# Optimization experiments

Hardware: AMD Instinct MI355X
Metric: run time of the kernel (lower is better)

The kernel has to match this reference:

```python
import jax, jax.numpy as jnp
import numpy as np

N_HEAD = 16
LORA_SCALE = 1.0 / 4.0  # alpha=1, r=4
LN_EPS = 1e-5


def _ln(x, g, b):
    # LayerNorm subclass casts to float32 then back to input dtype
    xf = x.astype(jnp.float32)
    m = xf.mean(-1, keepdims=True)
    v = xf.var(-1, keepdims=True)
    y = (xf - m) / jnp.sqrt(v + LN_EPS) * g + b
    return y.astype(x.dtype)


def _lora(h, a, b):
    # x @ a.T @ b.T * scaling ; a:[r,d], b:[d,r]
    return (h @ a.T) @ b.T * LORA_SCALE


def _attn(h, Wq, bq, Wk, Wv, bv, Wo, bo, la_k, lb_k, la_v, lb_v, la_o, lb_o):
    B, S, D = h.shape
    hd = D // N_HEAD
    scale = hd ** (-0.25)
    q = h @ Wq.T + bq
    k = h @ Wk.T + _lora(h, la_k, lb_k)          # key Linear has no bias
    v = h @ Wv.T + bv + _lora(h, la_v, lb_v)
    qh = q.reshape(B, S, N_HEAD, hd).transpose(0, 2, 1, 3) * scale  # [B,H,S,hd]
    kh = k.reshape(B, S, N_HEAD, hd).transpose(0, 2, 1, 3) * scale
    vh = v.reshape(B, S, N_HEAD, hd).transpose(0, 2, 1, 3)
    qk = jnp.einsum('bhqd,bhkd->bhqk', qh, kh).astype(jnp.float32)
    w = jax.nn.softmax(qk, axis=-1).astype(q.dtype)
    wv = jnp.einsum('bhqk,bhkd->bhqd', w, vh)
    wv = wv.transpose(0, 2, 1, 3).reshape(B, S, D)
    return wv @ Wo.T + bo + _lora(wv, la_o, lb_o)


def setup_inputs() -> dict:
    key = jax.random.key(0)
    D, R = 1024, 4
    B, S = 8, 1024
    ks = jax.random.split(key, 20)
    sd = 0.02
    inp = {
        'x': jax.random.normal(ks[0], (B, S, D), jnp.float32),
        'Wq': jax.random.normal(ks[1], (D, D), jnp.float32) * sd,
        'bq': jnp.zeros((D,), jnp.float32),
        'Wk': jax.random.normal(ks[2], (D, D), jnp.float32) * sd,
        'Wv': jax.random.normal(ks[3], (D, D), jnp.float32) * sd,
        'bv': jnp.zeros((D,), jnp.float32),
        'Wo': jax.random.normal(ks[4], (D, D), jnp.float32) * sd,
        'bo': jnp.zeros((D,), jnp.float32),
        'la_k': jax.random.normal(ks[5], (R, D), jnp.float32) * sd,
        'lb_k': jax.random.normal(ks[6], (D, R), jnp.float32) * sd,
        'la_v': jax.random.normal(ks[7], (R, D), jnp.float32) * sd,
        'lb_v': jax.random.normal(ks[8], (D, R), jnp.float32) * sd,
        'la_o': jax.random.normal(ks[9], (R, D), jnp.float32) * sd,
        'lb_o': jax.random.normal(ks[10], (D, R), jnp.float32) * sd,
        'g_attn': jnp.ones((D,), jnp.float32),
        'b_attn': jnp.zeros((D,), jnp.float32),
        'W1': jax.random.normal(ks[11], (4 * D, D), jnp.float32) * sd,
        'b1': jnp.zeros((4 * D,), jnp.float32),
        'W2': jax.random.normal(ks[12], (D, 4 * D), jnp.float32) * sd,
        'b2': jnp.zeros((D,), jnp.float32),
        'g_mlp': jnp.ones((D,), jnp.float32),
        'b_mlp': jnp.zeros((D,), jnp.float32),
    }
    return inp


def reference(x, Wq, bq, Wk, Wv, bv, Wo, bo, la_k, lb_k, la_v, lb_v, la_o, lb_o,
              g_attn, b_attn, W1, b1, W2, b2, g_mlp, b_mlp):
    # self-attention + residual (LoRA on key/value/out)
    x = x + _attn(_ln(x, g_attn, b_attn), Wq, bq, Wk, Wv, bv, Wo, bo,
                  la_k, lb_k, la_v, lb_v, la_o, lb_o)
    # MLP + residual (exact GELU, matching nn.GELU default)
    h = _ln(x, g_mlp, b_mlp)
    h = jax.nn.gelu(h @ W1.T + b1, approximate=False)
    x = x + h @ W2.T + b2
    return x
```

## Files before the change

### kernel.cpp

```cpp
#include <hip/hip_runtime.h>
#include <math.h>

typedef _Float16 f16_t;
typedef f16_t f16x8 __attribute__((ext_vector_type(8)));
typedef f16_t f16x4 __attribute__((ext_vector_type(4)));
typedef float f32x4 __attribute__((ext_vector_type(4)));
typedef float fv4 __attribute__((ext_vector_type(4)));

#define MFMA16(a, b, c) __builtin_amdgcn_mfma_f32_16x16x32_f16(a, b, c, 0, 0, 0)

__device__ __forceinline__ void gload16(const void* g, void* l) {
  __builtin_amdgcn_global_load_lds((const __attribute__((address_space(1))) void*)g,
                                   (__attribute__((address_space(3))) void*)l, 16, 0, 0);
}

__global__ __launch_bounds__(256) void ln_f32(const float* __restrict__ x,
                                              const float* __restrict__ g,
                                              const float* __restrict__ b,
                                              f16_t* __restrict__ y) {
  const int D = 1024;
  int row = blockIdx.x;
  int t = threadIdx.x;
  const float* xr = x + (size_t)row * D + t * 4;
  float x0 = xr[0], x1 = xr[1], x2 = xr[2], x3 = xr[3];
  float sum = x0 + x1 + x2 + x3;
  float sq = x0 * x0 + x1 * x1 + x2 * x2 + x3 * x3;
  for (int d = 32; d; d >>= 1) {
    sum += __shfl_down(sum, d);
    sq += __shfl_down(sq, d);
  }
  __shared__ float ssum[4], ssq[4];
  int w = t >> 6, lane = t & 63;
  if (lane == 0) { ssum[w] = sum; ssq[w] = sq; }
  __syncthreads();
  float ts = ssum[0] + ssum[1] + ssum[2] + ssum[3];
  float tq = ssq[0] + ssq[1] + ssq[2] + ssq[3];
  float mean = ts * (1.0f / 1024.0f);
  float var = tq * (1.0f / 1024.0f) - mean * mean;
  float rstd = rsqrtf(var + 1e-5f);
  f16_t* yr = y + (size_t)row * D + t * 4;
  const float* gr = g + t * 4;
  const float* br = b + t * 4;
  yr[0] = (f16_t)((x0 - mean) * rstd * gr[0] + br[0]);
  yr[1] = (f16_t)((x1 - mean) * rstd * gr[1] + br[1]);
  yr[2] = (f16_t)((x2 - mean) * rstd * gr[2] + br[2]);
  yr[3] = (f16_t)((x3 - mean) * rstd * gr[3] + br[3]);
}

__global__ __launch_bounds__(256) void ln_f16(const f16_t* __restrict__ x,
                                              const float* __restrict__ g,
                                              const float* __restrict__ b,
                                              f16_t* __restrict__ y) {
  const int D = 1024;
  int row = blockIdx.x;
  int t = threadIdx.x;
  const f16_t* xr = x + (size_t)row * D + t * 4;
  float x0 = (float)xr[0], x1 = (float)xr[1], x2 = (float)xr[2], x3 = (float)xr[3];
  float sum = x0 + x1 + x2 + x3;
  float sq = x0 * x0 + x1 * x1 + x2 * x2 + x3 * x3;
  for (int d = 32; d; d >>= 1) {
    sum += __shfl_down(sum, d);
    sq += __shfl_down(sq, d);
  }
  __shared__ float ssum[4], ssq[4];
  int w = t >> 6, lane = t & 63;
  if (lane == 0) { ssum[w] = sum; ssq[w] = sq; }
  __syncthreads();
  float ts = ssum[0] + ssum[1] + ssum[2] + ssum[3];
  float tq = ssq[0] + ssq[1] + ssq[2] + ssq[3];
  float mean = ts * (1.0f / 1024.0f);
  float var = tq * (1.0f / 1024.0f) - mean * mean;
  float rstd = rsqrtf(var + 1e-5f);
  f16_t* yr = y + (size_t)row * D + t * 4;
  const float* gr = g + t * 4;
  const float* br = b + t * 4;
  yr[0] = (f16_t)((x0 - mean) * rstd * gr[0] + br[0]);
  yr[1] = (f16_t)((x1 - mean) * rstd * gr[1] + br[1]);
  yr[2] = (f16_t)((x2 - mean) * rstd * gr[2] + br[2]);
  yr[3] = (f16_t)((x3 - mean) * rstd * gr[3] + br[3]);
}

__global__ __launch_bounds__(256) void convert_w(
    const float* __restrict__ wq, const float* __restrict__ wk,
    const float* __restrict__ wv, const float* __restrict__ wo,
    const float* __restrict__ w1, const float* __restrict__ w2,
    f16_t* __restrict__ oq, f16_t* __restrict__ ok, f16_t* __restrict__ ov,
    f16_t* __restrict__ oo, f16_t* __restrict__ o1, f16_t* __restrict__ o2) {
  int bid = blockIdx.x;
  const float* src;
  f16_t* dst;
  int bi;
  if (bid < 2048) {
    int seg = bid >> 9;
    bi = bid & 511;
    src = seg == 0 ? wq : seg == 1 ? wk : seg == 2 ? wv : wo;
    dst = seg == 0 ? oq : seg == 1 ? ok : seg == 2 ? ov : oo;
  } else if (bid < 4096) {
    bi = bid - 2048; src = w1; dst = o1;
  } else {
    bi = bid - 4096; src = w2; dst = o2;
  }
  size_t idx = (size_t)bi * 2048 + (size_t)threadIdx.x * 8;
  fv4 a = *(const fv4*)(src + idx);
  fv4 b = *(const fv4*)(src + idx + 4);
  f16x8 h;
#pragma unroll
  for (int j = 0; j < 4; ++j) { h[j] = (f16_t)a[j]; h[4 + j] = (f16_t)b[j]; }
  *(f16x8*)(dst + idx) = h;
}

__global__ __launch_bounds__(256) void lora_t_kernel(const f16_t* __restrict__ h,
                                                     const float* __restrict__ la,
                                                     float* __restrict__ t, int K) {
  int lane = threadIdx.x & 63;
  int w = threadIdx.x >> 6;
  int row = blockIdx.x * 4 + w;
  const f16_t* hrow = h + (size_t)row * K;
  float acc[4] = {0.f, 0.f, 0.f, 0.f};
  for (int it = 0; it < K / 512; ++it) {
    int base = it * 512 + lane * 8;
    f16x8 hx = *(const f16x8*)(hrow + base);
#pragma unroll
    for (int r = 0; r < 4; ++r) {
      const float* ar = la + (size_t)r * K + base;
#pragma unroll
      for (int j = 0; j < 8; ++j) acc[r] += (float)hx[j] * ar[j];
    }
  }
#pragma unroll
  for (int r = 0; r < 4; ++r) {
    for (int d = 32; d; d >>= 1) acc[r] += __shfl_down(acc[r], d);
  }
  if (lane == 0) {
#pragma unroll
    for (int r = 0; r < 4; ++r) t[(size_t)row * 4 + r] = acc[r];
  }
}

__global__ __launch_bounds__(256, 2) void gemm_f16(
    const f16_t* __restrict__ A, const f16_t* __restrict__ B,
    const float* __restrict__ bias, const float* __restrict__ loraT,
    const float* __restrict__ loraB, const float* residf,
    const f16_t* __restrict__ residb, f16_t* Cb, float* Cf, f16_t* Cvt,
    int M, int N, int K, int ldb, int dogelu) {
  __shared__ __align__(16) f16_t smem[2][16384];
  const int tid = threadIdx.x;
  const int lane = tid & 63, wid = tid >> 6;
  const int wm = wid >> 1, wn = wid & 1;
  const int l15 = lane & 15, lhi = lane >> 4;
  int nwg = gridDim.x * gridDim.y;
  int bid = blockIdx.y * gridDim.x + blockIdx.x;
  int swz = (bid & 7) * (nwg >> 3) + (bid >> 3);
  const int m0 = (swz / gridDim.x) * 128, n0 = (swz % gridDim.x) * 128;
  const int arow = tid >> 3;
  const int aslot = tid & 7;

  f32x4 acc[4][4];
#pragma unroll
  for (int i = 0; i < 4; ++i)
#pragma unroll
    for (int j = 0; j < 4; ++j) acc[i][j] = (f32x4){0.f, 0.f, 0.f, 0.f};

  auto stage = [&](const f16_t* G, int r0, int ldg, int step, char* lds) {
#pragma unroll
    for (int c = 0; c < 4; ++c) {
      int r = c * 32 + arow;
      int cm = aslot ^ (r & 7);
      gload16(G + (size_t)(r0 + r) * ldg + (size_t)step * 64 + cm * 8,
              lds + c * 4096 + wid * 1024);
    }
  };

  const int nsteps = K >> 6;
  stage(A, m0, K, 0, (char*)&smem[0][0]);
  stage(B, n0, ldb, 0, (char*)&smem[0][8192]);
  __syncthreads();
  for (int t = 0; t < nsteps; ++t) {
    int cur = t & 1, nxt = cur ^ 1;
    if (t + 1 < nsteps) {
      stage(A, m0, K, t + 1, (char*)&smem[nxt][0]);
      stage(B, n0, ldb, t + 1, (char*)&smem[nxt][8192]);
    }
    const char* As = (const char*)&smem[cur][0];
    const char* Bs = (const char*)&smem[cur][8192];
#pragma unroll
    for (int kk = 0; kk < 2; ++kk) {
      f16x8 af[4], bf[4];
#pragma unroll
      for (int i = 0; i < 4; ++i) {
        int row = wm * 64 + i * 16 + l15;
        af[i] = *(const f16x8*)(As + row * 128 + ((kk * 64 + lhi * 16) ^ ((row & 7) << 4)));
      }
#pragma unroll
      for (int j = 0; j < 4; ++j) {
        int row = wn * 64 + j * 16 + l15;
        bf[j] = *(const f16x8*)(Bs + row * 128 + ((kk * 64 + lhi * 16) ^ ((row & 7) << 4)));
      }
#pragma unroll
      for (int i = 0; i < 4; ++i)
#pragma unroll
        for (int j = 0; j < 4; ++j) acc[i][j] = MFMA16(af[i], bf[j], acc[i][j]);
    }
    __syncthreads();
  }

  const int gm = m0 + wm * 64, gn = n0 + wn * 64;
#pragma unroll
  for (int j = 0; j < 4; ++j) {
    int gcol = gn + j * 16 + l15;
    float bj = bias ? bias[gcol] : 0.f;
    float lb0 = 0.f, lb1 = 0.f, lb2 = 0.f, lb3 = 0.f;
    if (loraB) {
      const float* p = loraB + (size_t)gcol * 4;
      lb0 = p[0]; lb1 = p[1]; lb2 = p[2]; lb3 = p[3];
    }
#pragma unroll
    for (int i = 0; i < 4; ++i) {
      float v4[4];
#pragma unroll
      for (int r = 0; r < 4; ++r) {
        int grow = gm + i * 16 + lhi * 4 + r;
        float val = acc[i][j][r] + bj;
        if (loraT) {
          const float* tp = loraT + (size_t)grow * 4;
          val += 0.25f * (tp[0] * lb0 + tp[1] * lb1 + tp[2] * lb2 + tp[3] * lb3);
        }
        if (dogelu) val = 0.5f * val * (1.0f + erff(val * 0.70710678118654752f));
        if (residf) val += residf[(size_t)grow * N + gcol];
        if (residb) val += (float)residb[(size_t)grow * N + gcol];
        v4[r] = val;
      }
      if (Cf) {
#pragma unroll
        for (int r = 0; r < 4; ++r)
          Cf[(size_t)(gm + i * 16 + lhi * 4 + r) * N + gcol] = v4[r];
      } else if (Cvt) {
        int grow0 = gm + i * 16 + lhi * 4;
        int bb = grow0 >> 10, ss = grow0 & 1023;
        int hh = gcol >> 6, dd = gcol & 63;
        f16x4 pk;
#pragma unroll
        for (int r = 0; r < 4; ++r) pk[r] = (f16_t)v4[r];
        *(f16x4*)(Cvt + (((size_t)bb * 16 + hh) * 64 + dd) * 1024 + ss) = pk;
      } else {
#pragma unroll
        for (int r = 0; r < 4; ++r)
          Cb[(size_t)(gm + i * 16 + lhi * 4 + r) * N + gcol] = (f16_t)v4[r];
      }
    }
  }
}

__global__ __launch_bounds__(256, 2) void gemm_mfma(
    const f16_t* __restrict__ A, const float* __restrict__ B,
    const float* __restrict__ bias, const float* __restrict__ loraT,
    const float* __restrict__ loraB, const float* residf,
    const f16_t* __restrict__ residb, f16_t* Cb, float* Cf, f16_t* Cvt,
    int M, int N, int K, int ldb, int dogelu) {
  __shared__ __align__(16) f16_t smem[2][16384];
  const int tid = threadIdx.x;
  const int lane = tid & 63, wid = tid >> 6;
  const int wm = wid >> 1, wn = wid & 1;
  const int l15 = lane & 15, lhi = lane >> 4;
  const int m0 = blockIdx.y * 128, n0 = blockIdx.x * 128;
  const int arow = tid >> 3;
  const int aslot = tid & 7;

  f32x4 acc[4][4];
#pragma unroll
  for (int i = 0; i < 4; ++i)
#pragma unroll
    for (int j = 0; j < 4; ++j) acc[i][j] = (f32x4){0.f, 0.f, 0.f, 0.f};

  fv4 breg[4][2];

  auto stageA = [&](int step, int buf) {
#pragma unroll
    for (int c = 0; c < 4; ++c) {
      int r = c * 32 + arow;
      int cm = aslot ^ (r & 7);
      gload16(A + (size_t)(m0 + r) * K + (size_t)step * 64 + cm * 8,
              (char*)&smem[buf][0] + c * 4096 + wid * 1024);
    }
  };
  auto loadB = [&](int step) {
#pragma unroll
    for (int c = 0; c < 4; ++c) {
      int r = c * 32 + arow;
      const float* gp = B + (size_t)(n0 + r) * ldb + (size_t)step * 64 + aslot * 8;
      breg[c][0] = *(const fv4*)gp;
      breg[c][1] = *(const fv4*)(gp + 4);
    }
  };
  auto writeB = [&](int buf) {
#pragma unroll
    for (int c = 0; c < 4; ++c) {
      int r = c * 32 + arow;
      f16x8 hh;
#pragma unroll
      for (int j = 0; j < 4; ++j) hh[j] = (f16_t)breg[c][0][j];
#pragma unroll
      for (int j = 0; j < 4; ++j) hh[4 + j] = (f16_t)breg[c][1][j];
      int boff = r * 128 + ((aslot * 16) ^ ((r & 7) << 4));
      *(f16x8*)((char*)&smem[buf][8192] + boff) = hh;
    }
  };

  const int nsteps = K >> 6;
  stageA(0, 0);
  loadB(0);
  writeB(0);
  __syncthreads();
  for (int t = 0; t < nsteps; ++t) {
    int cur = t & 1, nxt = cur ^ 1;
    if (t + 1 < nsteps) { stageA(t + 1, nxt); loadB(t + 1); }
    const char* As = (const char*)&smem[cur][0];
    const char* Bs = (const char*)&smem[cur][8192];
#pragma unroll
    for (int kk = 0; kk < 2; ++kk) {
      f16x8 af[4], bf[4];
#pragma unroll
      for (int i = 0; i < 4; ++i) {
        int row = wm * 64 + i * 16 + l15;
        af[i] = *(const f16x8*)(As + row * 128 + ((kk * 64 + lhi * 16) ^ ((row & 7) << 4)));
      }
#pragma unroll
      for (int j = 0; j < 4; ++j) {
        int row = wn * 64 + j * 16 + l15;
        bf[j] = *(const f16x8*)(Bs + row * 128 + ((kk * 64 + lhi * 16) ^ ((row & 7) << 4)));
      }
#pragma unroll
      for (int i = 0; i < 4; ++i)
#pragma unroll
        for (int j = 0; j < 4; ++j) acc[i][j] = MFMA16(af[i], bf[j], acc[i][j]);
    }
    if (t + 1 < nsteps) writeB(nxt);
    __syncthreads();
  }

  const int gm = m0 + wm * 64, gn = n0 + wn * 64;
#pragma unroll
  for (int j = 0; j < 4; ++j) {
    int gcol = gn + j * 16 + l15;
    float bj = bias ? bias[gcol] : 0.f;
    float lb0 = 0.f, lb1 = 0.f, lb2 = 0.f, lb3 = 0.f;
    if (loraB) {
      const float* p = loraB + (size_t)gcol * 4;
      lb0 = p[0]; lb1 = p[1]; lb2 = p[2]; lb3 = p[3];
    }
#pragma unroll
    for (int i = 0; i < 4; ++i) {
      float v4[4];
#pragma unroll
      for (int r = 0; r < 4; ++r) {
        int grow = gm + i * 16 + lhi * 4 + r;
        float val = acc[i][j][r] + bj;
        if (loraT) {
          const float* tp = loraT + (size_t)grow * 4;
          val += 0.25f * (tp[0] * lb0 + tp[1] * lb1 + tp[2] * lb2 + tp[3] * lb3);
        }
        if (dogelu) val = 0.5f * val * (1.0f + erff(val * 0.70710678118654752f));
        if (residf) val += residf[(size_t)grow * N + gcol];
        if (residb) val += (float)residb[(size_t)grow * N + gcol];
        v4[r] = val;
      }
      if (Cf) {
#pragma unroll
        for (int r = 0; r < 4; ++r)
          Cf[(size_t)(gm + i * 16 + lhi * 4 + r) * N + gcol] = v4[r];
      } else if (Cvt) {
        int grow0 = gm + i * 16 + lhi * 4;
        int bb = grow0 >> 10, ss = grow0 & 1023;
        int hh = gcol >> 6, dd = gcol & 63;
        f16x4 pk;
#pragma unroll
        for (int r = 0; r < 4; ++r) pk[r] = (f16_t)v4[r];
        *(f16x4*)(Cvt + (((size_t)bb * 16 + hh) * 64 + dd) * 1024 + ss) = pk;
      } else {
#pragma unroll
        for (int r = 0; r < 4; ++r)
          Cb[(size_t)(gm + i * 16 + lhi * 4 + r) * N + gcol] = (f16_t)v4[r];
      }
    }
  }
}

__global__ __launch_bounds__(256, 3) void attn_mfma(const f16_t* __restrict__ q,
                                                    const f16_t* __restrict__ k,
                                                    const f16_t* __restrict__ vt,
                                                    f16_t* __restrict__ wv) {
  const int S = 1024, D = 1024;
  __shared__ __align__(16) f16_t Qs[128 * 64];
  __shared__ __align__(16) f16_t SP[128 * 64];
  __shared__ __align__(16) f16_t Ks[64 * 64];
  __shared__ __align__(16) f16_t Vts[64 * 64];
  __shared__ float rsb[128];
  __shared__ float lib[128];
  const int tid = threadIdx.x, lane = tid & 63, w = tid >> 6;
  const int l15 = lane & 15, lhi = lane >> 4;
  const int q0 = blockIdx.x * 128;
  const int h = blockIdx.y, b = blockIdx.z;
  const f16_t* qg = q + ((size_t)b * S + q0) * D + h * 64;
  const f16_t* kg = k + (size_t)b * S * D + h * 64;
  const f16_t* vg = vt + ((size_t)b * 16 + h) * 64 * (size_t)S;

#pragma unroll
  for (int c = 0; c < 4; ++c) {
    int r = c * 32 + (tid >> 3), kc = tid & 7;
    f16x8 xx = *(const f16x8*)(qg + (size_t)r * D + kc * 8);
    *(f16x8*)((char*)Qs + r * 128 + ((kc * 16) ^ ((r & 7) << 4))) = xx;
  }
  __syncthreads();
  f16x8 qf[2][2];
#pragma unroll
  for (int i = 0; i < 2; ++i) {
    int row = w * 32 + i * 16 + l15;
#pragma unroll
    for (int kk = 0; kk < 2; ++kk)
      qf[i][kk] = *(const f16x8*)((char*)Qs + row * 128 +
                                  ((kk * 64 + lhi * 16) ^ ((row & 7) << 4)));
  }

  f32x4 oacc[2][4];
#pragma unroll
  for (int i = 0; i < 2; ++i)
#pragma unroll
    for (int j = 0; j < 4; ++j) oacc[i][j] = (f32x4){0.f, 0.f, 0.f, 0.f};
  float m_run = -1e30f, l_run = 0.f;
  const int myrow = w * 32 + (lane >> 1);
  const int half = lane & 1;

  for (int kv = 0; kv < 16; ++kv) {
    __syncthreads();
#pragma unroll
    for (int c = 0; c < 2; ++c) {
      int r = c * 32 + (tid >> 3), kc = tid & 7;
      f16x8 xk = *(const f16x8*)(kg + (size_t)(kv * 64 + r) * D + kc * 8);
      *(f16x8*)((char*)Ks + r * 128 + ((kc * 16) ^ ((r & 7) << 4))) = xk;
      f16x8 xv = *(const f16x8*)(vg + (size_t)r * S + kv * 64 + kc * 8);
      *(f16x8*)((char*)Vts + r * 128 + ((kc * 16) ^ ((r & 7) << 4))) = xv;
    }
    __syncthreads();
    f32x4 sacc[2][4];
#pragma unroll
    for (int i = 0; i < 2; ++i)
#pragma unroll
      for (int j = 0; j < 4; ++j) sacc[i][j] = (f32x4){0.f, 0.f, 0.f, 0.f};
#pragma unroll
    for (int kk = 0; kk < 2; ++kk) {
      f16x8 kf[4];
#pragma unroll
      for (int j = 0; j < 4; ++j) {
        int row = j * 16 + l15;
        kf[j] = *(const f16x8*)((char*)Ks + row * 128 +
                                ((kk * 64 + lhi * 16) ^ ((row & 7) << 4)));
      }
#pragma unroll
      for (int i = 0; i < 2; ++i)
#pragma unroll
        for (int j = 0; j < 4; ++j) sacc[i][j] = MFMA16(qf[i][kk], kf[j], sacc[i][j]);
    }
#pragma unroll
    for (int i = 0; i < 2; ++i)
#pragma unroll
      for (int j = 0; j < 4; ++j)
#pragma unroll
        for (int r = 0; r < 4; ++r) {
          int srow = w * 32 + i * 16 + lhi * 4 + r;
          int scol = j * 16 + l15;
          *(f16_t*)((char*)SP + srow * 128 + ((scol * 2) ^ ((srow & 7) << 4))) =
              (f16_t)(sacc[i][j][r] * 0.125f);
        }
    __syncthreads();
    f16x8 ch[4];
#pragma unroll
    for (int c = 0; c < 4; ++c)
      ch[c] = *(const f16x8*)((char*)SP + myrow * 128 +
                              ((half * 64 + c * 16) ^ ((myrow & 7) << 4)));
    float mt = -1e30f;
#pragma unroll
    for (int c = 0; c < 4; ++c)
#pragma unroll
      for (int e = 0; e < 8; ++e) mt = fmaxf(mt, (float)ch[c][e]);
    mt = fmaxf(mt, __shfl_xor(mt, 1));
    float mnew = fmaxf(m_run, mt);
    float resc = __expf(m_run - mnew);
    float lsum = 0.f;
#pragma unroll
    for (int c = 0; c < 4; ++c) {
      f16x8 p8;
#pragma unroll
      for (int e = 0; e < 8; ++e) {
        float p = __expf((float)ch[c][e] - mnew);
        lsum += p;
        p8[e] = (f16_t)p;
      }
      *(f16x8*)((char*)SP + myrow * 128 + ((half * 64 + c * 16) ^ ((myrow & 7) << 4))) = p8;
    }
    lsum += __shfl_xor(lsum, 1);
    l_run = l_run * resc + lsum;
    m_run = mnew;
    if (half == 0) rsb[myrow] = resc;
    __syncthreads();
#pragma unroll
    for (int i = 0; i < 2; ++i) {
      float f0 = rsb[w * 32 + i * 16 + lhi * 4 + 0];
      float f1 = rsb[w * 32 + i * 16 + lhi * 4 + 1];
      float f2 = rsb[w * 32 + i * 16 + lhi * 4 + 2];
      float f3 = rsb[w * 32 + i * 16 + lhi * 4 + 3];
#pragma unroll
      for (int j = 0; j < 4; ++j) {
        oacc[i][j][0] *= f0;
        oacc[i][j][1] *= f1;
        oacc[i][j][2] *= f2;
        oacc[i][j][3] *= f3;
      }
    }
#pragma unroll
    for (int kk = 0; kk < 2; ++kk) {
      f16x8 pa[2], vb[4];
#pragma unroll
      for (int i = 0; i < 2; ++i) {
        int row = w * 32 + i * 16 + l15;
        pa[i] = *(const f16x8*)((char*)SP + row * 128 +
                                ((kk * 64 + lhi * 16) ^ ((row & 7) << 4)));
      }
#pragma unroll
      for (int j = 0; j < 4; ++j) {
        int row = j * 16 + l15;
        vb[j] = *(const f16x8*)((char*)Vts + row * 128 +
                                ((kk * 64 + lhi * 16) ^ ((row & 7) << 4)));
      }
#pragma unroll
      for (int i = 0; i < 2; ++i)
#pragma unroll
        for (int j = 0; j < 4; ++j) oacc[i][j] = MFMA16(pa[i], vb[j], oacc[i][j]);
    }
  }
  if (half == 0) lib[myrow] = 1.f / l_run;
  __syncthreads();
#pragma unroll
  for (int i = 0; i < 2; ++i)
#pragma unroll
    for (int r = 0; r < 4; ++r) {
      int row = w * 32 + i * 16 + lhi * 4 + r;
      float li = lib[row];
      size_t base = ((size_t)b * S + q0 + row) * D + h * 64;
#pragma unroll
      for (int j = 0; j < 4; ++j)
        wv[base + j * 16 + l15] = (f16_t)(oacc[i][j][r] * li);
    }
}

extern "C" void kernel_launch(void* const* d_in, const int* in_sizes, int n_in,
                              void* d_out, int out_size, void* d_ws, size_t ws_size,
                              hipStream_t stream) {
  const int B = 8, S = 1024, D = 1024, F = 4096;
  const int M = B * S;

  const float* x = (const float*)d_in[0];
  const float* Wq = (const float*)d_in[1];
  const float* bq = (const float*)d_in[2];
  const float* Wk = (const float*)d_in[3];
  const float* Wv = (const float*)d_in[4];
  const float* bv = (const float*)d_in[5];
  const float* Wo = (const float*)d_in[6];
  const float* bo = (const float*)d_in[7];
  const float* la_k = (const float*)d_in[8];
  const float* lb_k = (const float*)d_in[9];
  const float* la_v = (const float*)d_in[10];
  const float* lb_v = (const float*)d_in[11];
  const float* la_o = (const float*)d_in[12];
  const float* lb_o = (const float*)d_in[13];
  const float* g_attn = (const float*)d_in[14];
  const float* b_attn = (const float*)d_in[15];
  const float* W1 = (const float*)d_in[16];
  const float* b1 = (const float*)d_in[17];
  const float* W2 = (const float*)d_in[18];
  const float* b2 = (const float*)d_in[19];
  const float* g_mlp = (const float*)d_in[20];
  const float* b_mlp = (const float*)d_in[21];

  float* t_k = (float*)((char*)d_ws + 16);
  float* t_v = t_k + (size_t)M * 4;
  float* t_o = t_v + (size_t)M * 4;
  const size_t MD = (size_t)M * D;
  f16_t* P0 = (f16_t*)((char*)d_ws + 409600);
  f16_t* P1 = P0 + MD;
  f16_t* P2 = P0 + 2 * MD;
  f16_t* P3 = P0 + 3 * MD;
  f16_t* Wqf = P0 + 4 * MD;
  f16_t* Wkf = Wqf + (size_t)D * D;
  f16_t* Wvf = Wkf + (size_t)D * D;
  f16_t* Wof = Wvf + (size_t)D * D;
  f16_t* W1f = Wof + (size_t)D * D;
  f16_t* W2f = W1f + (size_t)F * D;
  float* outf = (float*)d_out;
  const size_t need = 409600 + 4 * MD * sizeof(f16_t) +
                      (4 * (size_t)D * D + 2 * (size_t)F * D) * sizeof(f16_t);
  const bool f16w = ws_size >= need;

  if (f16w)
    convert_w<<<6144, 256, 0, stream>>>(Wq, Wk, Wv, Wo, W1, W2,
                                        Wqf, Wkf, Wvf, Wof, W1f, W2f);

  ln_f32<<<M, 256, 0, stream>>>(x, g_attn, b_attn, P0);
  lora_t_kernel<<<M / 4, 256, 0, stream>>>(P0, la_k, t_k, D);
  lora_t_kernel<<<M / 4, 256, 0, stream>>>(P0, la_v, t_v, D);
  if (f16w) {
    gemm_f16<<<dim3(8, 64), 256, 0, stream>>>(
        P0, Wqf, bq, nullptr, nullptr, nullptr, nullptr, P1, nullptr, nullptr,
        M, D, D, D, 0);
    gemm_f16<<<dim3(8, 64), 256, 0, stream>>>(
        P0, Wkf, nullptr, t_k, lb_k, nullptr, nullptr, P2, nullptr, nullptr,
        M, D, D, D, 0);
    gemm_f16<<<dim3(8, 64), 256, 0, stream>>>(
        P0, Wvf, bv, t_v, lb_v, nullptr, nullptr, nullptr, nullptr, P3,
        M, D, D, D, 0);
  } else {
    gemm_mfma<<<dim3(8, 64), 256, 0, stream>>>(
        P0, Wq, bq, nullptr, nullptr, nullptr, nullptr, P1, nullptr, nullptr,
        M, D, D, D, 0);
    gemm_mfma<<<dim3(8, 64), 256, 0, stream>>>(
        P0, Wk, nullptr, t_k, lb_k, nullptr, nullptr, P2, nullptr, nullptr,
        M, D, D, D, 0);
    gemm_mfma<<<dim3(8, 64), 256, 0, stream>>>(
        P0, Wv, bv, t_v, lb_v, nullptr, nullptr, nullptr, nullptr, P3,
        M, D, D, D, 0);
  }
  attn_mfma<<<dim3(8, 16, 8), 256, 0, stream>>>(P1, P2, P3, P0);
  lora_t_kernel<<<M / 4, 256, 0, stream>>>(P0, la_o, t_o, D);
  if (f16w)
    gemm_f16<<<dim3(8, 64), 256, 0, stream>>>(
        P0, Wof, bo, t_o, lb_o, x, nullptr, P3, nullptr, nullptr, M, D, D, D, 0);
  else
    gemm_mfma<<<dim3(8, 64), 256, 0, stream>>>(
        P0, Wo, bo, t_o, lb_o, x, nullptr, P3, nullptr, nullptr, M, D, D, D, 0);
  ln_f16<<<M, 256, 0, stream>>>(P3, g_mlp, b_mlp, P0);
  if (f16w) {
    gemm_f16<<<dim3(16, 64), 256, 0, stream>>>(
        P0, W1f, b1, nullptr, nullptr, nullptr, nullptr, P1, nullptr, nullptr,
        M, 2048, D, D, 1);
    gemm_f16<<<dim3(8, 64), 256, 0, stream>>>(
        P1, W2f, b2, nullptr, nullptr, nullptr, P3, nullptr, outf, nullptr,
        M, D, 2048, F, 0);
    gemm_f16<<<dim3(16, 64), 256, 0, stream>>>(
        P0, W1f + (size_t)2048 * D, b1 + 2048, nullptr, nullptr, nullptr, nullptr,
        P1, nullptr, nullptr, M, 2048, D, D, 1);
    gemm_f16<<<dim3(8, 64), 256, 0, stream>>>(
        P1, W2f + 2048, nullptr, nullptr, nullptr, outf, nullptr, nullptr, outf,
        nullptr, M, D, 2048, F, 0);
  } else {
    gemm_mfma<<<dim3(16, 64), 256, 0, stream>>>(
        P0, W1, b1, nullptr, nullptr, nullptr, nullptr, P1, nullptr, nullptr,
        M, 2048, D, D, 1);
    gemm_mfma<<<dim3(8, 64), 256, 0, stream>>>(
        P1, W2, b2, nullptr, nullptr, nullptr, P3, nullptr, outf, nullptr,
        M, D, 2048, F, 0);
    gemm_mfma<<<dim3(16, 64), 256, 0, stream>>>(
        P0, W1 + (size_t)2048 * D, b1 + 2048, nullptr, nullptr, nullptr, nullptr,
        P1, nullptr, nullptr, M, 2048, D, D, 1);
    gemm_mfma<<<dim3(8, 64), 256, 0, stream>>>(
        P1, W2 + 2048, nullptr, nullptr, nullptr, outf, nullptr, nullptr, outf,
        nullptr, M, D, 2048, F, 0);
  }
}
```

Before: 662.5 us.

## Register-resident softmax in attention, single-buffer GEMM for occupancy, fuse LoRA K/V

The attention kernel now computes the online softmax directly on the MFMA accumulator registers, using lane shuffles for the row max and row sum. This removes the LDS round trip of scores, the extra barrier and the rescale broadcast buffers, and Q staging now reuses the P buffer to cut LDS use. setprio hints are added around the MFMA phases. The f16 GEMM drops double buffering to halve LDS and raises the launch bound to 3 blocks per SM, giving up overlap of loads and compute in exchange for occupancy. The two LoRA down-projection kernels are fused into one that reads the activations once.

```diff
diff --git a/kernel.cpp b/kernel.cpp
--- a/kernel.cpp
+++ b/kernel.cpp
@@ -109,6 +109,47 @@
   *(f16x8*)(dst + idx) = h;
 }
 
+__global__ __launch_bounds__(256) void lora_kv_kernel(
+    const f16_t* __restrict__ h, const float* __restrict__ la_k,
+    const float* __restrict__ la_v, float* __restrict__ t_k,
+    float* __restrict__ t_v, int K) {
+  int lane = threadIdx.x & 63;
+  int w = threadIdx.x >> 6;
+  int row = blockIdx.x * 4 + w;
+  const f16_t* hrow = h + (size_t)row * K;
+  float ak[4] = {0.f, 0.f, 0.f, 0.f};
+  float av[4] = {0.f, 0.f, 0.f, 0.f};
+  for (int it = 0; it < K / 512; ++it) {
+    int base = it * 512 + lane * 8;
+    f16x8 hx = *(const f16x8*)(hrow + base);
+#pragma unroll
+    for (int r = 0; r < 4; ++r) {
+      const float* kr = la_k + (size_t)r * K + base;
+      const float* vr = la_v + (size_t)r * K + base;
+#pragma unroll
+      for (int j = 0; j < 8; ++j) {
+        float hv = (float)hx[j];
+        ak[r] += hv * kr[j];
+        av[r] += hv * vr[j];
+      }
+    }
+  }
+#pragma unroll
+  for (int r = 0; r < 4; ++r) {
+    for (int d = 32; d; d >>= 1) {
+      ak[r] += __shfl_down(ak[r], d);
+      av[r] += __shfl_down(av[r], d);
+    }
+  }
+  if (lane == 0) {
+#pragma unroll
+    for (int r = 0; r < 4; ++r) {
+      t_k[(size_t)row * 4 + r] = ak[r];
+      t_v[(size_t)row * 4 + r] = av[r];
+    }
+  }
+}
+
 __global__ __launch_bounds__(256) void lora_t_kernel(const f16_t* __restrict__ h,
                                                      const float* __restrict__ la,
                                                      float* __restrict__ t, int K) {
@@ -137,13 +178,14 @@
   }
 }
 
-__global__ __launch_bounds__(256, 2) void gemm_f16(
+__global__ __launch_bounds__(256, 3) void gemm_f16(
     const f16_t* __restrict__ A, const f16_t* __restrict__ B,
     const float* __restrict__ bias, const float* __restrict__ loraT,
     const float* __restrict__ loraB, const float* residf,
     const f16_t* __restrict__ residb, f16_t* Cb, float* Cf, f16_t* Cvt,
     int M, int N, int K, int ldb, int dogelu) {
-  __shared__ __align__(16) f16_t smem[2][16384];
+  __shared__ __align__(16) f16_t Asm[8192];
+  __shared__ __align__(16) f16_t Bsm[8192];
   const int tid = threadIdx.x;
   const int lane = tid & 63, wid = tid >> 6;
   const int wm = wid >> 1, wn = wid & 1;
@@ -172,36 +214,31 @@
   };
 
   const int nsteps = K >> 6;
-  stage(A, m0, K, 0, (char*)&smem[0][0]);
-  stage(B, n0, ldb, 0, (char*)&smem[0][8192]);
-  __syncthreads();
   for (int t = 0; t < nsteps; ++t) {
-    int cur = t & 1, nxt = cur ^ 1;
-    if (t + 1 < nsteps) {
-      stage(A, m0, K, t + 1, (char*)&smem[nxt][0]);
-      stage(B, n0, ldb, t + 1, (char*)&smem[nxt][8192]);
-    }
-    const char* As = (const char*)&smem[cur][0];
-    const char* Bs = (const char*)&smem[cur][8192];
+    if (t) __syncthreads();
+    stage(A, m0, K, t, (char*)Asm);
+    stage(B, n0, ldb, t, (char*)Bsm);
+    __syncthreads();
 #pragma unroll
     for (int kk = 0; kk < 2; ++kk) {
       f16x8 af[4], bf[4];
 #pragma unroll
       for (int i = 0; i < 4; ++i) {
         int row = wm * 64 + i * 16 + l15;
-        af[i] = *(const f16x8*)(As + row * 128 + ((kk * 64 + lhi * 16) ^ ((row & 7) << 4)));
+        af[i] = *(const f16x8*)((char*)Asm + row * 128 +
+                                ((kk * 64 + lhi * 16) ^ ((row & 7) << 4)));
       }
 #pragma unroll
       for (int j = 0; j < 4; ++j) {
         int row = wn * 64 + j * 16 + l15;
-        bf[j] = *(const f16x8*)(Bs + row * 128 + ((kk * 64 + lhi * 16) ^ ((row & 7) << 4)));
+        bf[j] = *(const f16x8*)((char*)Bsm + row * 128 +
+                                ((kk * 64 + lhi * 16) ^ ((row & 7) << 4)));
       }
 #pragma unroll
       for (int i = 0; i < 4; ++i)
 #pragma unroll
         for (int j = 0; j < 4; ++j) acc[i][j] = MFMA16(af[i], bf[j], acc[i][j]);
     }
-    __syncthreads();
   }
 
   const int gm = m0 + wm * 64, gn = n0 + wn * 64;
@@ -390,12 +427,9 @@
                                                     const f16_t* __restrict__ vt,
                                                     f16_t* __restrict__ wv) {
   const int S = 1024, D = 1024;
-  __shared__ __align__(16) f16_t Qs[128 * 64];
   __shared__ __align__(16) f16_t SP[128 * 64];
   __shared__ __align__(16) f16_t Ks[64 * 64];
   __shared__ __align__(16) f16_t Vts[64 * 64];
-  __shared__ float rsb[128];
-  __shared__ float lib[128];
   const int tid = threadIdx.x, lane = tid & 63, w = tid >> 6;
   const int l15 = lane & 15, lhi = lane >> 4;
   const int q0 = blockIdx.x * 128;
@@ -408,7 +442,7 @@
   for (int c = 0; c < 4; ++c) {
     int r = c * 32 + (tid >> 3), kc = tid & 7;
     f16x8 xx = *(const f16x8*)(qg + (size_t)r * D + kc * 8);
-    *(f16x8*)((char*)Qs + r * 128 + ((kc * 16) ^ ((r & 7) << 4))) = xx;
+    *(f16x8*)((char*)SP + r * 128 + ((kc * 16) ^ ((r & 7) << 4))) = xx;
   }
   __syncthreads();
   f16x8 qf[2][2];
@@ -417,7 +451,7 @@
     int row = w * 32 + i * 16 + l15;
 #pragma unroll
     for (int kk = 0; kk < 2; ++kk)
-      qf[i][kk] = *(const f16x8*)((char*)Qs + row * 128 +
+      qf[i][kk] = *(const f16x8*)((char*)SP + row * 128 +
                                   ((kk * 64 + lhi * 16) ^ ((row & 7) << 4)));
   }
 
@@ -426,9 +460,11 @@
   for (int i = 0; i < 2; ++i)
 #pragma unroll
     for (int j = 0; j < 4; ++j) oacc[i][j] = (f32x4){0.f, 0.f, 0.f, 0.f};
-  float m_run = -1e30f, l_run = 0.f;
-  const int myrow = w * 32 + (lane >> 1);
-  const int half = lane & 1;
+  float m_run[2][4], l_run[2][4];
+#pragma unroll
+  for (int i = 0; i < 2; ++i)
+#pragma unroll
+    for (int r = 0; r < 4; ++r) { m_run[i][r] = -1e30f; l_run[i][r] = 0.f; }
 
   for (int kv = 0; kv < 16; ++kv) {
     __syncthreads();
@@ -446,6 +482,7 @@
     for (int i = 0; i < 2; ++i)
 #pragma unroll
       for (int j = 0; j < 4; ++j) sacc[i][j] = (f32x4){0.f, 0.f, 0.f, 0.f};
+    __builtin_amdgcn_s_setprio(1);
 #pragma unroll
     for (int kk = 0; kk < 2; ++kk) {
       f16x8 kf[4];
@@ -460,62 +497,42 @@
 #pragma unroll
         for (int j = 0; j < 4; ++j) sacc[i][j] = MFMA16(qf[i][kk], kf[j], sacc[i][j]);
     }
-#pragma unroll
-    for (int i = 0; i < 2; ++i)
-#pragma unroll
-      for (int j = 0; j < 4; ++j)
-#pragma unroll
-        for (int r = 0; r < 4; ++r) {
-          int srow = w * 32 + i * 16 + lhi * 4 + r;
-          int scol = j * 16 + l15;
-          *(f16_t*)((char*)SP + srow * 128 + ((scol * 2) ^ ((srow & 7) << 4))) =
-              (f16_t)(sacc[i][j][r] * 0.125f);
-        }
+    __builtin_amdgcn_s_setprio(0);
+#pragma unroll
+    for (int i = 0; i < 2; ++i) {
+#pragma unroll
+      for (int r = 0; r < 4; ++r) {
+        float s0 = sacc[i][0][r] * 0.125f, s1 = sacc[i][1][r] * 0.125f;
+        float s2 = sacc[i][2][r] * 0.125f, s3 = sacc[i][3][r] * 0.125f;
+        float mt = fmaxf(fmaxf(s0, s1), fmaxf(s2, s3));
+        mt = fmaxf(mt, __shfl_xor(mt, 1));
+        mt = fmaxf(mt, __shfl_xor(mt, 2));
+        mt = fmaxf(mt, __shfl_xor(mt, 4));
+        mt = fmaxf(mt, __shfl_xor(mt, 8));
+        float mnew = fmaxf(m_run[i][r], mt);
+        float resc = __expf(m_run[i][r] - mnew);
+        m_run[i][r] = mnew;
+        float p0 = __expf(s0 - mnew), p1 = __expf(s1 - mnew);
+        float p2 = __expf(s2 - mnew), p3 = __expf(s3 - mnew);
+        float ls = p0 + p1 + p2 + p3;
+        ls += __shfl_xor(ls, 1);
+        ls += __shfl_xor(ls, 2);
+        ls += __shfl_xor(ls, 4);
+        ls += __shfl_xor(ls, 8);
+        l_run[i][r] = l_run[i][r] * resc + ls;
+        int srow = w * 32 + i * 16 + lhi * 4 + r;
+        char* rp = (char*)SP + srow * 128;
+        int sw = (srow & 7) << 4;
+        *(f16_t*)(rp + ((l15 * 2) ^ sw)) = (f16_t)p0;
+        *(f16_t*)(rp + ((32 + l15 * 2) ^ sw)) = (f16_t)p1;
+        *(f16_t*)(rp + ((64 + l15 * 2) ^ sw)) = (f16_t)p2;
+        *(f16_t*)(rp + ((96 + l15 * 2) ^ sw)) = (f16_t)p3;
+#pragma unroll
+        for (int j = 0; j < 4; ++j) oacc[i][j][r] *= resc;
+      }
+    }
     __syncthreads();
-    f16x8 ch[4];
-#pragma unroll
-    for (int c = 0; c < 4; ++c)
-      ch[c] = *(const f16x8*)((char*)SP + myrow * 128 +
-                              ((half * 64 + c * 16) ^ ((myrow & 7) << 4)));
-    float mt = -1e30f;
-#pragma unroll
-    for (int c = 0; c < 4; ++c)
-#pragma unroll
-      for (int e = 0; e < 8; ++e) mt = fmaxf(mt, (float)ch[c][e]);
-    mt = fmaxf(mt, __shfl_xor(mt, 1));
-    float mnew = fmaxf(m_run, mt);
-    float resc = __expf(m_run - mnew);
-    float lsum = 0.f;
-#pragma unroll
-    for (int c = 0; c < 4; ++c) {
-      f16x8 p8;
-#pragma unroll
-      for (int e = 0; e < 8; ++e) {
-        float p = __expf((float)ch[c][e] - mnew);
-        lsum += p;
-        p8[e] = (f16_t)p;
-      }
-      *(f16x8*)((char*)SP + myrow * 128 + ((half * 64 + c * 16) ^ ((myrow & 7) << 4))) = p8;
-    }
-    lsum += __shfl_xor(lsum, 1);
-    l_run = l_run * resc + lsum;
-    m_run = mnew;
-    if (half == 0) rsb[myrow] = resc;
-    __syncthreads();
-#pragma unroll
-    for (int i = 0; i < 2; ++i) {
-      float f0 = rsb[w * 32 + i * 16 + lhi * 4 + 0];
-      float f1 = rsb[w * 32 + i * 16 + lhi * 4 + 1];
-      float f2 = rsb[w * 32 + i * 16 + lhi * 4 + 2];
-      float f3 = rsb[w * 32 + i * 16 + lhi * 4 + 3];
-#pragma unroll
-      for (int j = 0; j < 4; ++j) {
-        oacc[i][j][0] *= f0;
-        oacc[i][j][1] *= f1;
-        oacc[i][j][2] *= f2;
-        oacc[i][j][3] *= f3;
-      }
-    }
+    __builtin_amdgcn_s_setprio(1);
 #pragma unroll
     for (int kk = 0; kk < 2; ++kk) {
       f16x8 pa[2], vb[4];
@@ -536,15 +553,14 @@
 #pragma unroll
         for (int j = 0; j < 4; ++j) oacc[i][j] = MFMA16(pa[i], vb[j], oacc[i][j]);
     }
-  }
-  if (half == 0) lib[myrow] = 1.f / l_run;
-  __syncthreads();
+    __builtin_amdgcn_s_setprio(0);
+  }
 #pragma unroll
   for (int i = 0; i < 2; ++i)
 #pragma unroll
     for (int r = 0; r < 4; ++r) {
       int row = w * 32 + i * 16 + lhi * 4 + r;
-      float li = lib[row];
+      float li = 1.0f / l_run[i][r];
       size_t base = ((size_t)b * S + q0 + row) * D + h * 64;
 #pragma unroll
       for (int j = 0; j < 4; ++j)
@@ -605,8 +621,7 @@
                                         Wqf, Wkf, Wvf, Wof, W1f, W2f);
 
   ln_f32<<<M, 256, 0, stream>>>(x, g_attn, b_attn, P0);
-  lora_t_kernel<<<M / 4, 256, 0, stream>>>(P0, la_k, t_k, D);
-  lora_t_kernel<<<M / 4, 256, 0, stream>>>(P0, la_v, t_v, D);
+  lora_kv_kernel<<<M / 4, 256, 0, stream>>>(P0, la_k, la_v, t_k, t_v, D);
   if (f16w) {
     gemm_f16<<<dim3(8, 64), 256, 0, stream>>>(
         P0, Wqf, bq, nullptr, nullptr, nullptr, nullptr, P1, nullptr, nullptr,
```

Result: slower. 704.3 us (+6.3%).
